# Optimization experiments

Measured on AMD Instinct MI355X. Metric: run time of the kernel, lower is better.

## Reference

```python
import jax, jax.numpy as jnp
import numpy as np

DIM = 512
HEADS = 8
DIM_HEAD = 64
INNER = HEADS * DIM_HEAD  # 512
SCALE = DIM_HEAD ** -0.5


def setup_inputs() -> dict:
    key = jax.random.key(0)
    k1, k2, k3, k4, k5 = jax.random.split(key, 5)
    B, N = 4, 2048
    x = jax.random.normal(k1, (B, N, DIM), dtype=jnp.float32)
    # LayerNorm params
    ln_gamma = jnp.ones((DIM,), dtype=jnp.float32)
    ln_beta = jnp.zeros((DIM,), dtype=jnp.float32)
    # Linear weights (torch nn.Linear stores [out, in]; we keep [in, out] for x @ W)
    w_qkv = jax.random.normal(k2, (DIM, 3 * INNER), dtype=jnp.float32) * (DIM ** -0.5)
    w_out = jax.random.normal(k3, (INNER, DIM), dtype=jnp.float32) * (INNER ** -0.5)
    return {"x": x, "ln_gamma": ln_gamma, "ln_beta": ln_beta, "w_qkv": w_qkv, "w_out": w_out}


def _layernorm(x, gamma, beta, eps=1e-5):
    mu = jnp.mean(x, axis=-1, keepdims=True)
    var = jnp.var(x, axis=-1, keepdims=True)
    return (x - mu) * jax.lax.rsqrt(var + eps) * gamma + beta


def reference(x, ln_gamma, ln_beta, w_qkv, w_out):
    B, N, _ = x.shape
    h = _layernorm(x, ln_gamma, ln_beta)
    qkv = h @ w_qkv                                   # [B, N, 3*INNER]
    q, k, v = jnp.split(qkv, 3, axis=-1)
    def to_heads(t):
        return t.reshape(B, N, HEADS, DIM_HEAD).transpose(0, 2, 1, 3)  # b h n d
    q, k, v = to_heads(q), to_heads(k), to_heads(v)
    dots = jnp.einsum('bhnd,bhmd->bhnm', q, k) * SCALE
    attn = jax.nn.softmax(dots, axis=-1)
    out = jnp.einsum('bhnm,bhmd->bhnd', attn, v)
    out = out.transpose(0, 2, 1, 3).reshape(B, N, INNER)
    return out @ w_out
```

## Files before the change

kernel.cpp:

```cpp
#include <hip/hip_runtime.h>
#include <hip/hip_bf16.h>

#define B_ 4
#define SEQ 2048
#define DIM_ 512
#define DH 64
#define NQKV 1536
#define ROWS (B_*SEQ)
#define QSCALE 0.1803368801111204f
#define FRAG_PER_BH (SEQ * DH)

typedef short v8s __attribute__((ext_vector_type(8)));
typedef short v4sv __attribute__((ext_vector_type(4)));
typedef float v4f __attribute__((ext_vector_type(4)));
typedef unsigned v4u __attribute__((ext_vector_type(4)));

#define MFMA16(a,b,c) __builtin_amdgcn_mfma_f32_16x16x32_bf16((a),(b),(c),0,0,0)

static __device__ __forceinline__ short f2bf(float f) {
    union { __hip_bfloat16 h; short s; } u;
    u.h = __float2bfloat16(f);
    return u.s;
}

static __device__ __forceinline__ unsigned cvtpk(float lo, float hi) {
    unsigned r;
    asm("v_cvt_pk_bf16_f32 %0, %1, %2" : "=v"(r) : "v"(lo), "v"(hi));
    return r;
}

static __device__ __forceinline__ v8s as_v8s(v4u u) {
    union { v4u u; v8s s; } p;
    p.u = u;
    return p.s;
}

static __device__ __forceinline__ void gll16(const void* g, void* l) {
    __builtin_amdgcn_global_load_lds((const __attribute__((address_space(1))) void*)g,
                                     (__attribute__((address_space(3))) void*)l,
                                     16, 0, 0);
}

__global__ __launch_bounds__(256) void ln_kernel(const float* __restrict__ x,
                                                 const float* __restrict__ gamma,
                                                 const float* __restrict__ beta,
                                                 short* __restrict__ h) {
    int wave = threadIdx.x >> 6;
    int lane = threadIdx.x & 63;
    int row = (blockIdx.x << 2) + wave;
    const float* xr = x + (size_t)row * DIM_ + lane * 8;
    float4 a = *(const float4*)xr;
    float4 b = *(const float4*)(xr + 4);
    float v[8] = {a.x, a.y, a.z, a.w, b.x, b.y, b.z, b.w};
    float s = 0.f, ss = 0.f;
#pragma unroll
    for (int j = 0; j < 8; j++) { s += v[j]; ss += v[j] * v[j]; }
#pragma unroll
    for (int off = 1; off < 64; off <<= 1) {
        s += __shfl_xor(s, off, 64);
        ss += __shfl_xor(ss, off, 64);
    }
    float mean = s * (1.f / DIM_);
    float var = ss * (1.f / DIM_) - mean * mean;
    float rstd = rsqrtf(var + 1e-5f);
    const float* gr = gamma + lane * 8;
    const float* br = beta + lane * 8;
    float4 g0 = *(const float4*)gr, g1 = *(const float4*)(gr + 4);
    float4 b0 = *(const float4*)br, b1 = *(const float4*)(br + 4);
    float gg[8] = {g0.x, g0.y, g0.z, g0.w, g1.x, g1.y, g1.z, g1.w};
    float bb[8] = {b0.x, b0.y, b0.z, b0.w, b1.x, b1.y, b1.z, b1.w};
    v8s o;
#pragma unroll
    for (int j = 0; j < 8; j++) o[j] = f2bf((v[j] - mean) * rstd * gg[j] + bb[j]);
    *(v8s*)(h + (size_t)row * DIM_ + lane * 8) = o;
}

__global__ __launch_bounds__(256) void castw_kernel(const float* __restrict__ w,
                                                    short* __restrict__ wt,
                                                    int K, int Ntot, int scale_cols) {
    __shared__ float tile[64][65];
    int nb = Ntot >> 6;
    int k0 = (blockIdx.x / nb) << 6;
    int n0 = (blockIdx.x % nb) << 6;
    int tc = threadIdx.x & 63;
    int t4 = threadIdx.x >> 6;
#pragma unroll
    for (int i = 0; i < 16; i++) {
        int r = (t4 << 4) + i;
        float val = w[(size_t)(k0 + r) * Ntot + n0 + tc];
        if (n0 + tc < scale_cols) val *= QSCALE;
        tile[r][tc] = val;
    }
    __syncthreads();
#pragma unroll
    for (int i = 0; i < 16; i++) {
        int r = (t4 << 4) + i;
        wt[(size_t)(n0 + r) * K + k0 + tc] = f2bf(tile[tc][r]);
    }
}

template <int MODE>
__global__ __launch_bounds__(256, 3) void gemm_kernel(const short* __restrict__ A,
                                                      const short* __restrict__ Bt,
                                                      short* __restrict__ Qo,
                                                      short* __restrict__ Kf,
                                                      short* __restrict__ Vf,
                                                      float* __restrict__ out,
                                                      int Ntot) {
    __shared__ short lmem[2 * 128 * 64];
    short* lA = lmem;
    short* lB = lmem + 128 * 64;
    int nb = Ntot >> 7;
    int wid = ((int)(blockIdx.x & 7)) * ((int)gridDim.x >> 3) + ((int)blockIdx.x >> 3);
    int m0 = (wid / nb) << 7;
    int n0 = (wid % nb) << 7;
    int t = threadIdx.x;
    int wave = t >> 6, lane = t & 63;
    int ql = lane & 15, grp = lane >> 4;
    int wr = (wave >> 1) << 6, wc = (wave & 1) << 6;
    int srow = lane >> 3;
    int scol = ((lane & 7) ^ srow) << 3;
    const short* Asrc = A + (size_t)(m0 + (wave << 5) + srow) * DIM_ + scol;
    const short* Bsrc = Bt + (size_t)(n0 + (wave << 5) + srow) * DIM_ + scol;
    short* lAw = &lA[(wave << 5) << 6];
    short* lBw = &lB[(wave << 5) << 6];
    int swz = (ql & 7) << 3;
    v4f acc[4][4];
#pragma unroll
    for (int i = 0; i < 4; i++)
#pragma unroll
        for (int j = 0; j < 4; j++)
#pragma unroll
            for (int r = 0; r < 4; r++) acc[i][j][r] = 0.f;

    for (int k0 = 0; k0 < DIM_; k0 += 64) {
#pragma unroll
        for (int i = 0; i < 4; i++) {
            gll16(Asrc + k0 + (size_t)(i << 3) * DIM_, lAw + ((i << 3) << 6));
            gll16(Bsrc + k0 + (size_t)(i << 3) * DIM_, lBw + ((i << 3) << 6));
        }
        __syncthreads();
#pragma unroll
        for (int kk = 0; kk < 64; kk += 32) {
            v8s af[4], bfr[4];
#pragma unroll
            for (int ms = 0; ms < 4; ms++)
                af[ms] = *(const v8s*)&lA[((wr + (ms << 4) + ql) << 6) + ((kk + (grp << 3)) ^ swz)];
#pragma unroll
            for (int ns = 0; ns < 4; ns++)
                bfr[ns] = *(const v8s*)&lB[((wc + (ns << 4) + ql) << 6) + ((kk + (grp << 3)) ^ swz)];
#pragma unroll
            for (int ms = 0; ms < 4; ms++)
#pragma unroll
                for (int ns = 0; ns < 4; ns++)
                    acc[ms][ns] = MFMA16(af[ms], bfr[ns], acc[ms][ns]);
        }
        __syncthreads();
    }
    if (MODE == 1) {
#pragma unroll
        for (int ms = 0; ms < 4; ms++)
#pragma unroll
            for (int ns = 0; ns < 4; ns++)
#pragma unroll
                for (int r = 0; r < 4; r++) {
                    int m = m0 + wr + (ms << 4) + (grp << 2) + r;
                    int n = n0 + wc + (ns << 4) + ql;
                    out[(size_t)m * DIM_ + n] = acc[ms][ns][r];
                }
    } else if (n0 < 512) {
#pragma unroll
        for (int ms = 0; ms < 4; ms++)
#pragma unroll
            for (int ns = 0; ns < 4; ns++)
#pragma unroll
                for (int r = 0; r < 4; r++) {
                    int m = m0 + wr + (ms << 4) + (grp << 2) + r;
                    int n = n0 + wc + (ns << 4) + ql;
                    int head = (n >> 6) & 7;
                    int d = n & 63;
                    int b = m >> 11;
                    int nseq = m & 2047;
                    size_t bh = (size_t)((b << 3) + head);
                    Qo[(bh * SEQ + nseq) * DH + d] = f2bf(acc[ms][ns][r]);
                }
    } else if (n0 < 1024) {
#pragma unroll
        for (int ms = 0; ms < 4; ms++)
#pragma unroll
            for (int ns = 0; ns < 4; ns++)
#pragma unroll
                for (int r = 0; r < 4; r++) {
                    int m = m0 + wr + (ms << 4) + (grp << 2) + r;
                    int n = n0 + wc + (ns << 4) + ql;
                    int head = (n >> 6) & 7;
                    int d = n & 63;
                    int b = m >> 11;
                    int nseq = m & 2047;
                    int tl = nseq >> 6, p = nseq & 63;
                    int pp = (p & 32) | (((p >> 2) & 1) << 4) | (((p >> 4) & 1) << 3)
                           | (((p >> 3) & 1) << 2) | (p & 3);
                    int tt = pp >> 4, qlk = pp & 15;
                    int hh = d >> 5, grpk = (d >> 3) & 3, j = d & 7;
                    size_t bh = (size_t)((b << 3) + head);
                    Kf[bh * FRAG_PER_BH +
                       ((((size_t)(tl * 4 + tt) * 2 + hh) * 64 + grpk * 16 + qlk) << 3) + j] =
                        f2bf(acc[ms][ns][r]);
                }
    } else {
#pragma unroll
        for (int ms = 0; ms < 4; ms++)
#pragma unroll
            for (int ns = 0; ns < 4; ns++) {
                int seq0 = (m0 & 2047) + wr + (ms << 4) + (grp << 2);
                int tl = seq0 >> 6, s = seq0 & 63;
                int g = s >> 5, grpv = (s >> 3) & 3, j0 = s & 7;
                int n = n0 + wc + (ns << 4) + ql;
                int head = (n >> 6) & 7;
                int d = n & 63;
                int ds = d >> 4, qlv = d & 15;
                int b = m0 >> 11;
                size_t bh = (size_t)((b << 3) + head);
                v4sv o;
#pragma unroll
                for (int r = 0; r < 4; r++) o[r] = f2bf(acc[ms][ns][r]);
                *(v4sv*)&Vf[bh * FRAG_PER_BH +
                            ((((size_t)(tl * 2 + g) * 4 + ds) * 64 + grpv * 16 + qlv) << 3) + j0] = o;
            }
    }
}

__global__ __launch_bounds__(512) void attn_kernel(const short* __restrict__ Q,
                                                   const short* __restrict__ Kf,
                                                   const short* __restrict__ Vf,
                                                   short* __restrict__ aout) {
    int tid = threadIdx.x;
    int wave = tid >> 6, lane = tid & 63;
    int ql = lane & 15, grp = lane >> 4;
    int wid = (((int)blockIdx.x & 7) << 5) + ((int)blockIdx.x >> 3);
    int bh = wid >> 3;
    int q0 = (wid & 7) << 8;
    const short* Qb = Q + (size_t)bh * SEQ * DH;
    const short* Kb = Kf + (size_t)bh * FRAG_PER_BH;
    const short* Vb = Vf + (size_t)bh * FRAG_PER_BH;
    int l16 = lane << 3;

    v8s qf[2][2];
#pragma unroll
    for (int qs = 0; qs < 2; qs++) {
        const short* qrow = Qb + (size_t)(q0 + (wave << 5) + (qs << 4) + ql) * DH + (grp << 3);
        qf[qs][0] = *(const v8s*)qrow;
        qf[qs][1] = *(const v8s*)(qrow + 32);
    }

    v4f oacc[2][4];
#pragma unroll
    for (int qs = 0; qs < 2; qs++)
#pragma unroll
        for (int i = 0; i < 4; i++)
#pragma unroll
            for (int r = 0; r < 4; r++) oacc[qs][i][r] = 0.f;
    float plocal[2] = {0.f, 0.f};

    v8s kcur[8];
#pragma unroll
    for (int f = 0; f < 8; f++) kcur[f] = *(const v8s*)&Kb[(f << 9) + l16];

    for (int t = 0; t < SEQ / 64; t++) {
        v8s vcur[8];
#pragma unroll
        for (int f = 0; f < 8; f++)
            vcur[f] = *(const v8s*)&Vb[(t << 12) + (f << 9) + l16];
        v4f sacc[2][4];
#pragma unroll
        for (int qs = 0; qs < 2; qs++)
#pragma unroll
            for (int i = 0; i < 4; i++)
#pragma unroll
                for (int r = 0; r < 4; r++) sacc[qs][i][r] = 0.f;
        __builtin_amdgcn_s_setprio(1);
#pragma unroll
        for (int tt = 0; tt < 4; tt++)
#pragma unroll
            for (int qs = 0; qs < 2; qs++) {
                sacc[qs][tt] = MFMA16(kcur[(tt << 1)], qf[qs][0], sacc[qs][tt]);
                sacc[qs][tt] = MFMA16(kcur[(tt << 1) + 1], qf[qs][1], sacc[qs][tt]);
            }
        __builtin_amdgcn_s_setprio(0);
        v8s knext[8];
        if (t < SEQ / 64 - 1) {
#pragma unroll
            for (int f = 0; f < 8; f++)
                knext[f] = *(const v8s*)&Kb[((t + 1) << 12) + (f << 9) + l16];
        }
        v4u pk[2][2];
#pragma unroll
        for (int qs = 0; qs < 2; qs++)
#pragma unroll
            for (int tt = 0; tt < 4; tt++) {
                float e0 = exp2f(sacc[qs][tt][0]);
                float e1 = exp2f(sacc[qs][tt][1]);
                float e2 = exp2f(sacc[qs][tt][2]);
                float e3 = exp2f(sacc[qs][tt][3]);
                plocal[qs] += (e0 + e1) + (e2 + e3);
                pk[qs][tt >> 1][(tt & 1) << 1] = cvtpk(e0, e1);
                pk[qs][tt >> 1][((tt & 1) << 1) + 1] = cvtpk(e2, e3);
            }
        __builtin_amdgcn_s_setprio(1);
#pragma unroll
        for (int g = 0; g < 2; g++)
#pragma unroll
            for (int qs = 0; qs < 2; qs++) {
                v8s pf = as_v8s(pk[qs][g]);
#pragma unroll
                for (int ds = 0; ds < 4; ds++)
                    oacc[qs][ds] = MFMA16(vcur[(g << 2) + ds], pf, oacc[qs][ds]);
            }
        __builtin_amdgcn_s_setprio(0);
        if (t < SEQ / 64 - 1) {
#pragma unroll
            for (int f = 0; f < 8; f++) kcur[f] = knext[f];
        }
    }
    int b = bh >> 3, head = bh & 7;
#pragma unroll
    for (int qs = 0; qs < 2; qs++) {
        float p = plocal[qs];
        p += __shfl_xor(p, 16, 64);
        p += __shfl_xor(p, 32, 64);
        float inv = 1.f / p;
        int n = q0 + (wave << 5) + (qs << 4) + ql;
        size_t rowbase = ((size_t)(b * SEQ + n)) * DIM_ + (head << 6);
#pragma unroll
        for (int ds = 0; ds < 4; ds++) {
            v4sv o;
#pragma unroll
            for (int r = 0; r < 4; r++) o[r] = f2bf(oacc[qs][ds][r] * inv);
            *(v4sv*)&aout[rowbase + (ds << 4) + (grp << 2)] = o;
        }
    }
}

extern "C" void kernel_launch(void* const* d_in, const int* in_sizes, int n_in,
                              void* d_out, int out_size, void* d_ws, size_t ws_size,
                              hipStream_t stream) {
    const float* x = (const float*)d_in[0];
    const float* gamma = (const float*)d_in[1];
    const float* beta = (const float*)d_in[2];
    const float* w_qkv = (const float*)d_in[3];
    const float* w_out = (const float*)d_in[4];
    float* out = (float*)d_out;

    short* ws = (short*)d_ws;
    short* h = ws;
    short* wqkvT = h + (size_t)ROWS * DIM_;
    short* woutT = wqkvT + (size_t)NQKV * DIM_;
    short* Qb = woutT + (size_t)DIM_ * DIM_;
    short* Kfb = Qb + (size_t)32 * SEQ * DH;
    short* Vfb = Kfb + (size_t)32 * SEQ * DH;
    short* aout = Vfb + (size_t)32 * SEQ * DH;

    hipLaunchKernelGGL(ln_kernel, dim3(ROWS / 4), dim3(256), 0, stream, x, gamma, beta, h);
    hipLaunchKernelGGL(castw_kernel, dim3((DIM_ / 64) * (NQKV / 64)), dim3(256), 0, stream,
                       w_qkv, wqkvT, DIM_, NQKV, 512);
    hipLaunchKernelGGL(castw_kernel, dim3((DIM_ / 64) * (DIM_ / 64)), dim3(256), 0, stream,
                       w_out, woutT, DIM_, DIM_, 0);
    hipLaunchKernelGGL((gemm_kernel<0>), dim3((ROWS / 128) * (NQKV / 128)), dim3(256), 0, stream,
                       h, wqkvT, Qb, Kfb, Vfb, (float*)nullptr, NQKV);
    hipLaunchKernelGGL(attn_kernel, dim3(32 * 8), dim3(512), 0, stream, Qb, Kfb, Vfb, aout);
    hipLaunchKernelGGL((gemm_kernel<1>), dim3((ROWS / 128) * (DIM_ / 128)), dim3(256), 0, stream,
                       aout, woutT, (short*)nullptr, (short*)nullptr, (short*)nullptr, out, DIM_);
}
```

Before: 102.4 us.

## Double query rows per wave and ping-pong K prefetch in attention

Each attention wave now processes 64 query rows instead of 32, halving the per-row K/V fragment loads from global memory, and blocks shrink to 4 waves. The K prefetch is issued before the QK MFMAs and alternates between two register arrays via a 2x-unrolled loop, removing the register copy. Register pressure roughly doubles for accumulators, which risks lower occupancy or spills, and fewer waves per CU reduce latency hiding.

```diff
diff --git a/kernel.cpp b/kernel.cpp
--- a/kernel.cpp
+++ b/kernel.cpp
@@ -230,7 +230,7 @@
     }
 }
 
-__global__ __launch_bounds__(512) void attn_kernel(const short* __restrict__ Q,
+__global__ __launch_bounds__(256) void attn_kernel(const short* __restrict__ Q,
                                                    const short* __restrict__ Kf,
                                                    const short* __restrict__ Vf,
                                                    short* __restrict__ aout) {
@@ -245,91 +245,94 @@
     const short* Vb = Vf + (size_t)bh * FRAG_PER_BH;
     int l16 = lane << 3;
 
-    v8s qf[2][2];
-#pragma unroll
-    for (int qs = 0; qs < 2; qs++) {
-        const short* qrow = Qb + (size_t)(q0 + (wave << 5) + (qs << 4) + ql) * DH + (grp << 3);
+    v8s qf[4][2];
+#pragma unroll
+    for (int qs = 0; qs < 4; qs++) {
+        const short* qrow = Qb + (size_t)(q0 + (wave << 6) + (qs << 4) + ql) * DH + (grp << 3);
         qf[qs][0] = *(const v8s*)qrow;
         qf[qs][1] = *(const v8s*)(qrow + 32);
     }
 
-    v4f oacc[2][4];
-#pragma unroll
-    for (int qs = 0; qs < 2; qs++)
+    v4f oacc[4][4];
+#pragma unroll
+    for (int qs = 0; qs < 4; qs++)
 #pragma unroll
         for (int i = 0; i < 4; i++)
 #pragma unroll
             for (int r = 0; r < 4; r++) oacc[qs][i][r] = 0.f;
-    float plocal[2] = {0.f, 0.f};
-
-    v8s kcur[8];
-#pragma unroll
-    for (int f = 0; f < 8; f++) kcur[f] = *(const v8s*)&Kb[(f << 9) + l16];
-
-    for (int t = 0; t < SEQ / 64; t++) {
-        v8s vcur[8];
-#pragma unroll
-        for (int f = 0; f < 8; f++)
-            vcur[f] = *(const v8s*)&Vb[(t << 12) + (f << 9) + l16];
-        v4f sacc[2][4];
-#pragma unroll
-        for (int qs = 0; qs < 2; qs++)
-#pragma unroll
-            for (int i = 0; i < 4; i++)
-#pragma unroll
-                for (int r = 0; r < 4; r++) sacc[qs][i][r] = 0.f;
-        __builtin_amdgcn_s_setprio(1);
-#pragma unroll
-        for (int tt = 0; tt < 4; tt++)
-#pragma unroll
-            for (int qs = 0; qs < 2; qs++) {
-                sacc[qs][tt] = MFMA16(kcur[(tt << 1)], qf[qs][0], sacc[qs][tt]);
-                sacc[qs][tt] = MFMA16(kcur[(tt << 1) + 1], qf[qs][1], sacc[qs][tt]);
-            }
-        __builtin_amdgcn_s_setprio(0);
-        v8s knext[8];
-        if (t < SEQ / 64 - 1) {
-#pragma unroll
-            for (int f = 0; f < 8; f++)
-                knext[f] = *(const v8s*)&Kb[((t + 1) << 12) + (f << 9) + l16];
-        }
-        v4u pk[2][2];
-#pragma unroll
-        for (int qs = 0; qs < 2; qs++)
-#pragma unroll
-            for (int tt = 0; tt < 4; tt++) {
-                float e0 = exp2f(sacc[qs][tt][0]);
-                float e1 = exp2f(sacc[qs][tt][1]);
-                float e2 = exp2f(sacc[qs][tt][2]);
-                float e3 = exp2f(sacc[qs][tt][3]);
-                plocal[qs] += (e0 + e1) + (e2 + e3);
-                pk[qs][tt >> 1][(tt & 1) << 1] = cvtpk(e0, e1);
-                pk[qs][tt >> 1][((tt & 1) << 1) + 1] = cvtpk(e2, e3);
-            }
-        __builtin_amdgcn_s_setprio(1);
-#pragma unroll
-        for (int g = 0; g < 2; g++)
-#pragma unroll
-            for (int qs = 0; qs < 2; qs++) {
-                v8s pf = as_v8s(pk[qs][g]);
-#pragma unroll
-                for (int ds = 0; ds < 4; ds++)
-                    oacc[qs][ds] = MFMA16(vcur[(g << 2) + ds], pf, oacc[qs][ds]);
-            }
-        __builtin_amdgcn_s_setprio(0);
-        if (t < SEQ / 64 - 1) {
-#pragma unroll
-            for (int f = 0; f < 8; f++) kcur[f] = knext[f];
-        }
-    }
+    float plocal[4] = {0.f, 0.f, 0.f, 0.f};
+
+    v8s kA[8], kB[8];
+#pragma unroll
+    for (int f = 0; f < 8; f++) kA[f] = *(const v8s*)&Kb[(f << 9) + l16];
+
+#define ATTN_TILE(T, KC, KN)                                                            \
+    {                                                                                   \
+        v8s vcur[8];                                                                    \
+        _Pragma("unroll")                                                               \
+        for (int f = 0; f < 8; f++)                                                     \
+            vcur[f] = *(const v8s*)&Vb[((T) << 12) + (f << 9) + l16];                   \
+        if ((T) + 1 < SEQ / 64) {                                                       \
+            _Pragma("unroll")                                                           \
+            for (int f = 0; f < 8; f++)                                                 \
+                KN[f] = *(const v8s*)&Kb[(((T) + 1) << 12) + (f << 9) + l16];           \
+        }                                                                               \
+        v4f sacc[4][4];                                                                 \
+        _Pragma("unroll")                                                               \
+        for (int qs = 0; qs < 4; qs++)                                                  \
+            _Pragma("unroll")                                                           \
+            for (int i = 0; i < 4; i++)                                                 \
+                _Pragma("unroll")                                                       \
+                for (int r = 0; r < 4; r++) sacc[qs][i][r] = 0.f;                       \
+        __builtin_amdgcn_s_setprio(1);                                                  \
+        _Pragma("unroll")                                                               \
+        for (int tt = 0; tt < 4; tt++)                                                  \
+            _Pragma("unroll")                                                           \
+            for (int qs = 0; qs < 4; qs++) {                                            \
+                sacc[qs][tt] = MFMA16(KC[(tt << 1)], qf[qs][0], sacc[qs][tt]);          \
+                sacc[qs][tt] = MFMA16(KC[(tt << 1) + 1], qf[qs][1], sacc[qs][tt]);      \
+            }                                                                           \
+        __builtin_amdgcn_s_setprio(0);                                                  \
+        v4u pk[4][2];                                                                   \
+        _Pragma("unroll")                                                               \
+        for (int qs = 0; qs < 4; qs++)                                                  \
+            _Pragma("unroll")                                                           \
+            for (int tt = 0; tt < 4; tt++) {                                            \
+                float e0 = exp2f(sacc[qs][tt][0]);                                      \
+                float e1 = exp2f(sacc[qs][tt][1]);                                      \
+                float e2 = exp2f(sacc[qs][tt][2]);                                      \
+                float e3 = exp2f(sacc[qs][tt][3]);                                      \
+                plocal[qs] += (e0 + e1) + (e2 + e3);                                    \
+                pk[qs][tt >> 1][(tt & 1) << 1] = cvtpk(e0, e1);                         \
+                pk[qs][tt >> 1][((tt & 1) << 1) + 1] = cvtpk(e2, e3);                   \
+            }                                                                           \
+        __builtin_amdgcn_s_setprio(1);                                                  \
+        _Pragma("unroll")                                                               \
+        for (int g = 0; g < 2; g++)                                                     \
+            _Pragma("unroll")                                                           \
+            for (int qs = 0; qs < 4; qs++) {                                            \
+                v8s pf = as_v8s(pk[qs][g]);                                             \
+                _Pragma("unroll")                                                       \
+                for (int ds = 0; ds < 4; ds++)                                          \
+                    oacc[qs][ds] = MFMA16(vcur[(g << 2) + ds], pf, oacc[qs][ds]);       \
+            }                                                                           \
+        __builtin_amdgcn_s_setprio(0);                                                  \
+    }
+
+    for (int t = 0; t < SEQ / 64; t += 2) {
+        ATTN_TILE(t, kA, kB);
+        ATTN_TILE(t + 1, kB, kA);
+    }
+#undef ATTN_TILE
+
     int b = bh >> 3, head = bh & 7;
 #pragma unroll
-    for (int qs = 0; qs < 2; qs++) {
+    for (int qs = 0; qs < 4; qs++) {
         float p = plocal[qs];
         p += __shfl_xor(p, 16, 64);
         p += __shfl_xor(p, 32, 64);
         float inv = 1.f / p;
-        int n = q0 + (wave << 5) + (qs << 4) + ql;
+        int n = q0 + (wave << 6) + (qs << 4) + ql;
         size_t rowbase = ((size_t)(b * SEQ + n)) * DIM_ + (head << 6);
 #pragma unroll
         for (int ds = 0; ds < 4; ds++) {
@@ -367,7 +370,7 @@
                        w_out, woutT, DIM_, DIM_, 0);
     hipLaunchKernelGGL((gemm_kernel<0>), dim3((ROWS / 128) * (NQKV / 128)), dim3(256), 0, stream,
                        h, wqkvT, Qb, Kfb, Vfb, (float*)nullptr, NQKV);
-    hipLaunchKernelGGL(attn_kernel, dim3(32 * 8), dim3(512), 0, stream, Qb, Kfb, Vfb, aout);
+    hipLaunchKernelGGL(attn_kernel, dim3(32 * 8), dim3(256), 0, stream, Qb, Kfb, Vfb, aout);
     hipLaunchKernelGGL((gemm_kernel<1>), dim3((ROWS / 128) * (DIM_ / 128)), dim3(256), 0, stream,
                        aout, woutT, (short*)nullptr, (short*)nullptr, (short*)nullptr, out, DIM_);
 }
```

New measurement: 121.1 us. 18.3% more time.

## Split attention KV range across two wave halves and combine partials in LDS

Applied to the files above, without the earlier changes.

Each attention block now handles 128 query rows instead of 256. Its 8 waves form 4 query groups × 2 KV halves, and each half processes 16 of the 32 KV tiles. Partial outputs and row sums from the second half are written to shared memory and added by the first half before normalisation. This doubles the grid to 512 blocks so more CUs are busy and each wave's serial loop is shorter, at the cost of an LDS round-trip, a block barrier, and Q loads duplicated across the two halves. It also zero-initialises the score MFMA through a constant accumulator instead of clearing registers each iteration.

```diff
diff --git a/kernel.cpp b/kernel.cpp
--- a/kernel.cpp
+++ b/kernel.cpp
@@ -230,16 +230,18 @@
     }
 }
 
-__global__ __launch_bounds__(512) void attn_kernel(const short* __restrict__ Q,
-                                                   const short* __restrict__ Kf,
-                                                   const short* __restrict__ Vf,
-                                                   short* __restrict__ aout) {
+__global__ __launch_bounds__(512, 4) void attn_kernel(const short* __restrict__ Q,
+                                                      const short* __restrict__ Kf,
+                                                      const short* __restrict__ Vf,
+                                                      short* __restrict__ aout) {
+    __shared__ float lcomb[4 * 2112];
     int tid = threadIdx.x;
     int wave = tid >> 6, lane = tid & 63;
     int ql = lane & 15, grp = lane >> 4;
-    int wid = (((int)blockIdx.x & 7) << 5) + ((int)blockIdx.x >> 3);
-    int bh = wid >> 3;
-    int q0 = (wid & 7) << 8;
+    int qg = wave & 3, half = wave >> 2;
+    int wid = (((int)blockIdx.x & 7) << 6) + ((int)blockIdx.x >> 3);
+    int bh = wid >> 4;
+    int q0 = (wid & 15) << 7;
     const short* Qb = Q + (size_t)bh * SEQ * DH;
     const short* Kb = Kf + (size_t)bh * FRAG_PER_BH;
     const short* Vb = Vf + (size_t)bh * FRAG_PER_BH;
@@ -248,7 +250,7 @@
     v8s qf[2][2];
 #pragma unroll
     for (int qs = 0; qs < 2; qs++) {
-        const short* qrow = Qb + (size_t)(q0 + (wave << 5) + (qs << 4) + ql) * DH + (grp << 3);
+        const short* qrow = Qb + (size_t)(q0 + (qg << 5) + (qs << 4) + ql) * DH + (grp << 3);
         qf[qs][0] = *(const v8s*)qrow;
         qf[qs][1] = *(const v8s*)(qrow + 32);
     }
@@ -261,34 +263,30 @@
 #pragma unroll
             for (int r = 0; r < 4; r++) oacc[qs][i][r] = 0.f;
     float plocal[2] = {0.f, 0.f};
-
+    const v4f vzero = {0.f, 0.f, 0.f, 0.f};
+
+    int t0 = half << 4, t1 = t0 + 16;
     v8s kcur[8];
 #pragma unroll
-    for (int f = 0; f < 8; f++) kcur[f] = *(const v8s*)&Kb[(f << 9) + l16];
-
-    for (int t = 0; t < SEQ / 64; t++) {
+    for (int f = 0; f < 8; f++) kcur[f] = *(const v8s*)&Kb[(t0 << 12) + (f << 9) + l16];
+
+    for (int t = t0; t < t1; t++) {
         v8s vcur[8];
 #pragma unroll
         for (int f = 0; f < 8; f++)
             vcur[f] = *(const v8s*)&Vb[(t << 12) + (f << 9) + l16];
         v4f sacc[2][4];
-#pragma unroll
-        for (int qs = 0; qs < 2; qs++)
-#pragma unroll
-            for (int i = 0; i < 4; i++)
-#pragma unroll
-                for (int r = 0; r < 4; r++) sacc[qs][i][r] = 0.f;
         __builtin_amdgcn_s_setprio(1);
 #pragma unroll
         for (int tt = 0; tt < 4; tt++)
 #pragma unroll
             for (int qs = 0; qs < 2; qs++) {
-                sacc[qs][tt] = MFMA16(kcur[(tt << 1)], qf[qs][0], sacc[qs][tt]);
+                sacc[qs][tt] = MFMA16(kcur[(tt << 1)], qf[qs][0], vzero);
                 sacc[qs][tt] = MFMA16(kcur[(tt << 1) + 1], qf[qs][1], sacc[qs][tt]);
             }
         __builtin_amdgcn_s_setprio(0);
         v8s knext[8];
-        if (t < SEQ / 64 - 1) {
+        if (t + 1 < t1) {
 #pragma unroll
             for (int f = 0; f < 8; f++)
                 knext[f] = *(const v8s*)&Kb[((t + 1) << 12) + (f << 9) + l16];
@@ -317,26 +315,49 @@
                     oacc[qs][ds] = MFMA16(vcur[(g << 2) + ds], pf, oacc[qs][ds]);
             }
         __builtin_amdgcn_s_setprio(0);
-        if (t < SEQ / 64 - 1) {
+        if (t + 1 < t1) {
 #pragma unroll
             for (int f = 0; f < 8; f++) kcur[f] = knext[f];
         }
     }
-    int b = bh >> 3, head = bh & 7;
+    float pred[2];
 #pragma unroll
     for (int qs = 0; qs < 2; qs++) {
         float p = plocal[qs];
         p += __shfl_xor(p, 16, 64);
         p += __shfl_xor(p, 32, 64);
-        float inv = 1.f / p;
-        int n = q0 + (wave << 5) + (qs << 4) + ql;
-        size_t rowbase = ((size_t)(b * SEQ + n)) * DIM_ + (head << 6);
-#pragma unroll
-        for (int ds = 0; ds < 4; ds++) {
-            v4sv o;
-#pragma unroll
-            for (int r = 0; r < 4; r++) o[r] = f2bf(oacc[qs][ds][r] * inv);
-            *(v4sv*)&aout[rowbase + (ds << 4) + (grp << 2)] = o;
+        pred[qs] = p;
+    }
+    float* cb = &lcomb[qg * 2112];
+    if (half == 1) {
+#pragma unroll
+        for (int qs = 0; qs < 2; qs++) {
+#pragma unroll
+            for (int ds = 0; ds < 4; ds++)
+#pragma unroll
+                for (int r = 0; r < 4; r++)
+                    cb[((qs << 4) + ql) * 65 + (ds << 4) + (grp << 2) + r] = oacc[qs][ds][r];
+            if (grp == 0) cb[32 * 65 + (qs << 4) + ql] = pred[qs];
+        }
+    }
+    __syncthreads();
+    if (half == 0) {
+        int b = bh >> 3, head = bh & 7;
+#pragma unroll
+        for (int qs = 0; qs < 2; qs++) {
+            float ptot = pred[qs] + cb[32 * 65 + (qs << 4) + ql];
+            float inv = 1.f / ptot;
+            int n = q0 + (qg << 5) + (qs << 4) + ql;
+            size_t rowbase = ((size_t)(b * SEQ + n)) * DIM_ + (head << 6);
+#pragma unroll
+            for (int ds = 0; ds < 4; ds++) {
+                v4sv o;
+#pragma unroll
+                for (int r = 0; r < 4; r++)
+                    o[r] = f2bf((oacc[qs][ds][r] +
+                                 cb[((qs << 4) + ql) * 65 + (ds << 4) + (grp << 2) + r]) * inv);
+                *(v4sv*)&aout[rowbase + (ds << 4) + (grp << 2)] = o;
+            }
         }
     }
 }
@@ -367,7 +388,7 @@
                        w_out, woutT, DIM_, DIM_, 0);
     hipLaunchKernelGGL((gemm_kernel<0>), dim3((ROWS / 128) * (NQKV / 128)), dim3(256), 0, stream,
                        h, wqkvT, Qb, Kfb, Vfb, (float*)nullptr, NQKV);
-    hipLaunchKernelGGL(attn_kernel, dim3(32 * 8), dim3(512), 0, stream, Qb, Kfb, Vfb, aout);
+    hipLaunchKernelGGL(attn_kernel, dim3(32 * 16), dim3(512), 0, stream, Qb, Kfb, Vfb, aout);
     hipLaunchKernelGGL((gemm_kernel<1>), dim3((ROWS / 128) * (DIM_ / 128)), dim3(256), 0, stream,
                        aout, woutT, (short*)nullptr, (short*)nullptr, (short*)nullptr, out, DIM_);
 }
```

Measured after the change: 400.7 us. 291% more time.
